# Performance work log

Hardware: AMD Instinct MI355X
Metric: run time of the kernel (lower is better)

The kernel has to match this reference:

```python
import jax, jax.numpy as jnp
import numpy as np

D_MODEL = 512
NHEAD = 8
HEAD_DIM = D_MODEL // NHEAD
D_FF = 2048
EPS = 1e-5


def _linear_params(key, d_in, d_out):
    kw, kb = jax.random.split(key)
    bound = 1.0 / np.sqrt(d_in)
    W = jax.random.uniform(kw, (d_out, d_in), jnp.float32, -bound, bound)
    b = jax.random.uniform(kb, (d_out,), jnp.float32, -bound, bound)
    return W, b


def setup_inputs() -> dict:
    key = jax.random.key(0)
    ks = jax.random.split(key, 8)
    src = jax.random.normal(ks[0], (4, 2048, D_MODEL), jnp.float32)
    Wq, bq = _linear_params(ks[1], D_MODEL, D_MODEL)
    Wk, bk = _linear_params(ks[2], D_MODEL, D_MODEL)
    Wv, bv = _linear_params(ks[3], D_MODEL, D_MODEL)
    Wo, bo = _linear_params(ks[4], D_MODEL, D_MODEL)
    W1, b1 = _linear_params(ks[5], D_MODEL, D_FF)
    W2, b2 = _linear_params(ks[6], D_FF, D_MODEL)
    g1 = jnp.ones((D_MODEL,), jnp.float32)
    be1 = jnp.zeros((D_MODEL,), jnp.float32)
    g2 = jnp.ones((D_MODEL,), jnp.float32)
    be2 = jnp.zeros((D_MODEL,), jnp.float32)
    return dict(src=src, Wq=Wq, bq=bq, Wk=Wk, bk=bk, Wv=Wv, bv=bv,
                Wo=Wo, bo=bo, W1=W1, b1=b1, W2=W2, b2=b2,
                g1=g1, be1=be1, g2=g2, be2=be2)


def _layer_norm(x, g, b):
    mu = jnp.mean(x, axis=-1, keepdims=True)
    var = jnp.mean(jnp.square(x - mu), axis=-1, keepdims=True)
    return (x - mu) / jnp.sqrt(var + EPS) * g + b


def reference(src, Wq, bq, Wk, bk, Wv, bv, Wo, bo, W1, b1, W2, b2, g1, be1, g2, be2):
    B, T, D = src.shape
    scale = np.sqrt(HEAD_DIM).astype(np.float32)
    # Projections (torch Linear: x @ W.T + b)
    Q = (src @ Wq.T + bq).reshape(B, T, NHEAD, HEAD_DIM).transpose(0, 2, 1, 3)
    K = (src @ Wk.T + bk).reshape(B, T, NHEAD, HEAD_DIM).transpose(0, 2, 1, 3)
    V = (src @ Wv.T + bv).reshape(B, T, NHEAD, HEAD_DIM).transpose(0, 2, 1, 3)
    # Explicit QK^T -> softmax -> V (no mask, dropout=0)
    scores = jnp.einsum('bhqd,bhkd->bhqk', Q, K) / scale  # (B,H,T,T)
    attn = jax.nn.softmax(scores, axis=-1)
    ctx = jnp.einsum('bhqk,bhkd->bhqd', attn, V)
    ctx = ctx.transpose(0, 2, 1, 3).reshape(B, T, D)
    attn_out = ctx @ Wo.T + bo
    # Add & Norm 1
    x = _layer_norm(src + attn_out, g1, be1)
    # FFN: Linear -> GELU -> Linear
    h = jax.nn.gelu(x @ W1.T + b1, approximate=False)
    ffn_out = h @ W2.T + b2
    # Add & Norm 2
    return _layer_norm(x + ffn_out, g2, be2)
```

## Files before the change

### kernel.cpp

```cpp
#include <hip/hip_runtime.h>
#include <hip/hip_bf16.h>
#include <hip/hip_fp16.h>
#include <math.h>

typedef __bf16 bf16_t;
typedef __bf16 bf16x8 __attribute__((ext_vector_type(8)));
typedef __bf16 bf16x2 __attribute__((ext_vector_type(2)));
typedef float  f32x4  __attribute__((ext_vector_type(4)));

#define D_MODEL 512
#define NHEAD   8
#define HD      64
#define D_FF    2048
#define TOKENS  8192
#define SEQ     2048
#define BATCH   4

__device__ __forceinline__ void gload16(const bf16_t* g, bf16_t* l)
{
    __builtin_amdgcn_global_load_lds(
        (const __attribute__((address_space(1))) void*)g,
        (__attribute__((address_space(3))) void*)l,
        16, 0, 0);
}

__device__ __forceinline__ void cvt4(const float* s, bf16_t* d)
{
    float4 v = *(const float4*)s;
    alignas(8) bf16_t t[4] = {(bf16_t)v.x, (bf16_t)v.y, (bf16_t)v.z, (bf16_t)v.w};
    *(uint2*)d = *(const uint2*)t;
}

__global__ void cvt_weights(const float* __restrict__ src,
                            const float* __restrict__ Wq, const float* __restrict__ Wk,
                            const float* __restrict__ Wv, const float* __restrict__ Wo,
                            const float* __restrict__ W1, const float* __restrict__ W2,
                            const float* __restrict__ bq, const float* __restrict__ bk,
                            const float* __restrict__ bv,
                            bf16_t* __restrict__ Xb,
                            bf16_t* __restrict__ Wqkvb, bf16_t* __restrict__ Wob,
                            bf16_t* __restrict__ W1b, bf16_t* __restrict__ W2b,
                            float* __restrict__ bqkv, float* __restrict__ zbias)
{
    int i = blockIdx.x * 256 + threadIdx.x;
    if (i < 1048576) { cvt4(src + (size_t)i * 4, Xb + (size_t)i * 4); return; }
    i -= 1048576;
    if (i < 65536)        cvt4(Wq + (size_t)i * 4,            Wqkvb + (size_t)i * 4);
    else if (i < 131072)  cvt4(Wk + (size_t)(i - 65536) * 4,  Wqkvb + (size_t)i * 4);
    else if (i < 196608)  cvt4(Wv + (size_t)(i - 131072) * 4, Wqkvb + (size_t)i * 4);
    else if (i < 262144)  cvt4(Wo + (size_t)(i - 196608) * 4, Wob + (size_t)(i - 196608) * 4);
    else if (i < 524288)  cvt4(W1 + (size_t)(i - 262144) * 4, W1b + (size_t)(i - 262144) * 4);
    else if (i < 786432)  cvt4(W2 + (size_t)(i - 524288) * 4, W2b + (size_t)(i - 524288) * 4);
    else if (i < 786816) {
        int j = i - 786432;
        const float* s = (j < 128) ? bq + j * 4 : (j < 256) ? bk + (j - 128) * 4
                                                            : bv + (j - 256) * 4;
        *(float4*)(bqkv + (j & 127) * 4 + (j >> 7) * 512) = *(const float4*)s;
    } else if (i < 786944) {
        int j = i - 786816;
        *(float4*)(zbias + j * 4) = make_float4(0.f, 0.f, 0.f, 0.f);
    }
}

template <int BM, int EPI, bool SPLIT2>
__global__ __launch_bounds__(256)
void gemm_bt(const bf16_t* __restrict__ A, const bf16_t* __restrict__ B,
             const float* __restrict__ bias, const float* __restrict__ biasz,
             void* __restrict__ Cout, int M, int N, int K)
{
    constexpr int MI = BM / 32;
    __shared__ bf16_t sA[2][BM][32];
    __shared__ bf16_t sB[2][128][32];
    bf16_t* sAf = &sA[0][0][0];
    bf16_t* sBf = &sB[0][0][0];

    const int tid  = threadIdx.x;
    const int wave = tid >> 6;
    const int lane = tid & 63;
    const int g    = lane >> 4;
    const int c16  = lane & 15;
    const int wm   = (wave >> 1) * (BM / 2);
    const int wn   = (wave & 1) * 64;
    const int m0   = blockIdx.y * BM;
    const int n0   = blockIdx.x * 128;

    const int zz    = SPLIT2 ? blockIdx.z : 0;
    const int Keff  = SPLIT2 ? (K >> 1) : K;
    const int kbase = zz * Keff;
    const float* bptr = (SPLIT2 && zz) ? biasz : bias;

    const f32x4 fz = {0.f, 0.f, 0.f, 0.f};
    f32x4 acc[MI][4];
#pragma unroll
    for (int i = 0; i < MI; i++)
#pragma unroll
        for (int j = 0; j < 4; j++) acc[i][j] = fz;

    const int srow = tid >> 2;
    const int scol = (tid & 3) * 8;
    const bf16_t* pa = A + (size_t)(m0 + srow) * K + kbase + scol;
    const bf16_t* pb = B + (size_t)(n0 + srow) * K + kbase + scol;

#pragma unroll
    for (int i = 0; i < BM / 64; i++)
        gload16(pa + (size_t)i * 64 * K, sAf + i * 2048 + tid * 8);
#pragma unroll
    for (int i = 0; i < 2; i++)
        gload16(pb + (size_t)i * 64 * K, sBf + i * 2048 + tid * 8);

    const int NK = Keff >> 5;
    for (int kk = 0; kk < NK; ++kk) {
        const int cur = kk & 1;
        __syncthreads();
        if (kk + 1 < NK) {
            const int k0 = (kk + 1) * 32;
            bf16_t* dA = sAf + (cur ^ 1) * (BM * 32);
            bf16_t* dB = sBf + (cur ^ 1) * 4096;
#pragma unroll
            for (int i = 0; i < BM / 64; i++)
                gload16(pa + (size_t)i * 64 * K + k0, dA + i * 2048 + tid * 8);
#pragma unroll
            for (int i = 0; i < 2; i++)
                gload16(pb + (size_t)i * 64 * K + k0, dB + i * 2048 + tid * 8);
        }

        bf16x8 af[MI], bfr[4];
#pragma unroll
        for (int i = 0; i < MI; i++)
            af[i] = *(const bf16x8*)&sA[cur][wm + i * 16 + c16][g * 8];
#pragma unroll
        for (int j = 0; j < 4; j++)
            bfr[j] = *(const bf16x8*)&sB[cur][wn + j * 16 + c16][g * 8];
#pragma unroll
        for (int mi = 0; mi < MI; mi++)
#pragma unroll
            for (int ni = 0; ni < 4; ni++)
                acc[mi][ni] = __builtin_amdgcn_mfma_f32_16x16x32_bf16(
                    af[mi], bfr[ni], acc[mi][ni], 0, 0, 0);
    }

    __half* outh = (__half*)Cout + (size_t)zz * M * N;
#pragma unroll
    for (int mi = 0; mi < MI; mi++) {
#pragma unroll
        for (int ni = 0; ni < 4; ni++) {
            const int col = n0 + wn + ni * 16 + c16;
            const float bv = bptr[col];
#pragma unroll
            for (int r = 0; r < 4; r++) {
                const int row = m0 + wm + mi * 16 + g * 4 + r;
                float v = acc[mi][ni][r] + bv;
                if (EPI == 1) v = 0.5f * v * (1.f + erff(v * 0.70710678118654752f));
                if (EPI == 2)
                    outh[(size_t)row * N + col] = (__half)v;
                else
                    ((bf16_t*)Cout)[(size_t)row * N + col] = (bf16_t)v;
            }
        }
    }
}

__global__ __launch_bounds__(256)
void transpose_v(const bf16_t* __restrict__ qkv, bf16_t* __restrict__ vt)
{
    __shared__ bf16_t st[64][72];
    const int t0 = blockIdx.x * 64;
    const int bh = blockIdx.y;
    const int b = bh >> 3, h = bh & 7;
    const int tid = threadIdx.x;

    for (int c = tid; c < 512; c += 256) {
        int r = c >> 3, cj = (c & 7) * 8;
        const bf16_t* src = qkv + ((size_t)(b * SEQ + t0 + r)) * 1536 + 1024 + h * 64 + cj;
        *(int4*)&st[r][cj] = *(const int4*)src;
    }
    __syncthreads();
    for (int c = tid; c < 512; c += 256) {
        int d = c >> 3, pj = (c & 7) * 8;
        alignas(16) bf16_t tmp[8];
#pragma unroll
        for (int j = 0; j < 8; j++) {
            int p = pj + j;
            int t = (p & 32) + ((p & 1) << 4) + ((p & 31) >> 1);
            tmp[j] = st[t][d];
        }
        *(int4*)(vt + ((size_t)(bh * 64 + d)) * SEQ + t0 + pj) = *(const int4*)tmp;
    }
}

__global__ __launch_bounds__(256)
void flash_attn(const bf16_t* __restrict__ qkv, const bf16_t* __restrict__ vt,
                bf16_t* __restrict__ ctx)
{
    __shared__ bf16_t sK[2][64][64];
    __shared__ bf16_t sVt[2][64][64];
    __shared__ bf16_t sP[128][64];

    const int bh = blockIdx.y;
    const int b = bh >> 3, h = bh & 7;
    const int q0 = blockIdx.x * 128;
    const int tid = threadIdx.x;
    const int wave = tid >> 6, lane = tid & 63;
    const int g = lane >> 4, c16 = lane & 15;

    const float qscale = 0.125f * 1.4426950408889634f;
    bf16x8 aq[2][2];
#pragma unroll
    for (int mf = 0; mf < 2; mf++)
#pragma unroll
        for (int ks = 0; ks < 2; ks++) {
            bf16x8 v = *(const bf16x8*)(qkv +
                ((size_t)(b * SEQ + q0 + wave * 32 + mf * 16 + c16)) * 1536 +
                h * 64 + ks * 32 + g * 8);
#pragma unroll
            for (int j = 0; j < 8; j++) v[j] = (bf16_t)((float)v[j] * qscale);
            aq[mf][ks] = v;
        }

    bf16x8 vb_ones;
    {
        const bf16_t o = (bf16_t)((c16 == 0) ? 1.0f : 0.0f);
#pragma unroll
        for (int j = 0; j < 8; j++) vb_ones[j] = o;
    }

    const f32x4 fz = {0.f, 0.f, 0.f, 0.f};
    f32x4 acc_o[2][5];
#pragma unroll
    for (int mf = 0; mf < 2; mf++)
#pragma unroll
        for (int nd = 0; nd < 5; nd++) acc_o[mf][nd] = fz;

    const int f0 = tid,        r0 = f0 >> 3, l0 = (f0 & 7) ^ (r0 & 7);
    const int f1 = tid + 256,  r1 = f1 >> 3, l1 = (f1 & 7) ^ (r1 & 7);
    const bf16_t* gK0 = qkv + ((size_t)(b * SEQ + r0)) * 1536 + 512 + h * 64 + l0 * 8;
    const bf16_t* gK1 = qkv + ((size_t)(b * SEQ + r1)) * 1536 + 512 + h * 64 + l1 * 8;
    const bf16_t* gV0 = vt + ((size_t)(bh * 64 + r0)) * SEQ + l0 * 8;
    const bf16_t* gV1 = vt + ((size_t)(bh * 64 + r1)) * SEQ + l1 * 8;
    bf16_t* lK = &sK[0][0][0];
    bf16_t* lV = &sVt[0][0][0];

    gload16(gK0, lK + f0 * 8);
    gload16(gK1, lK + f1 * 8);
    gload16(gV0, lV + f0 * 8);
    gload16(gV1, lV + f1 * 8);

    for (int it = 0; it < 32; ++it) {
        const int cur = it & 1;
        __syncthreads();
        if (it < 31) {
            const size_t kv = (size_t)(it + 1) * 64;
            const int bo = (cur ^ 1) * 4096;
            gload16(gK0 + kv * 1536, lK + bo + f0 * 8);
            gload16(gK1 + kv * 1536, lK + bo + f1 * 8);
            gload16(gV0 + kv,        lV + bo + f0 * 8);
            gload16(gV1 + kv,        lV + bo + f1 * 8);
        }

        f32x4 accs[2][4];
#pragma unroll
        for (int mf = 0; mf < 2; mf++)
#pragma unroll
            for (int n = 0; n < 4; n++) accs[mf][n] = fz;
#pragma unroll
        for (int ks = 0; ks < 2; ks++)
#pragma unroll
            for (int n = 0; n < 4; n++) {
                const int pc = ((ks * 4 + g) ^ (c16 & 7)) * 8;
                bf16x8 bk = *(const bf16x8*)&sK[cur][n * 16 + c16][pc];
                accs[0][n] = __builtin_amdgcn_mfma_f32_16x16x32_bf16(aq[0][ks], bk, accs[0][n], 0, 0, 0);
                accs[1][n] = __builtin_amdgcn_mfma_f32_16x16x32_bf16(aq[1][ks], bk, accs[1][n], 0, 0, 0);
            }

#pragma unroll
        for (int mf = 0; mf < 2; mf++)
#pragma unroll
            for (int r = 0; r < 4; r++) {
                const int prow = wave * 32 + mf * 16 + g * 4 + r;
#pragma unroll
                for (int ks = 0; ks < 2; ks++) {
                    bf16x2 pp;
                    pp[0] = (bf16_t)__builtin_amdgcn_exp2f(accs[mf][2 * ks][r]);
                    pp[1] = (bf16_t)__builtin_amdgcn_exp2f(accs[mf][2 * ks + 1][r]);
                    const int lc = ks * 4 + (c16 >> 2);
                    const int pc = ((lc ^ (prow & 7)) << 3) + ((2 * c16) & 7);
                    *(bf16x2*)&sP[prow][pc] = pp;
                }
            }

#pragma unroll
        for (int ks = 0; ks < 2; ks++) {
            const int rpc = ((ks * 4 + g) ^ (c16 & 7)) * 8;
            bf16x8 ap0 = *(const bf16x8*)&sP[wave * 32 + c16][rpc];
            bf16x8 ap1 = *(const bf16x8*)&sP[wave * 32 + 16 + c16][rpc];
#pragma unroll
            for (int nd = 0; nd < 5; nd++) {
                bf16x8 vb;
                if (nd < 4) {
                    const int pc = ((ks * 4 + g) ^ (c16 & 7)) * 8;
                    vb = *(const bf16x8*)&sVt[cur][nd * 16 + c16][pc];
                } else {
                    vb = vb_ones;
                }
                acc_o[0][nd] = __builtin_amdgcn_mfma_f32_16x16x32_bf16(ap0, vb, acc_o[0][nd], 0, 0, 0);
                acc_o[1][nd] = __builtin_amdgcn_mfma_f32_16x16x32_bf16(ap1, vb, acc_o[1][nd], 0, 0, 0);
            }
        }
    }

#pragma unroll
    for (int mf = 0; mf < 2; mf++)
#pragma unroll
        for (int r = 0; r < 4; r++) {
            float lv  = __shfl(acc_o[mf][4][r], lane & 48, 64);
            float inv = 1.0f / lv;
            const size_t base =
                ((size_t)(b * SEQ + q0 + wave * 32 + mf * 16 + g * 4 + r)) * 512 + h * 64;
#pragma unroll
            for (int nd = 0; nd < 4; nd++)
                ctx[base + nd * 16 + c16] = (bf16_t)(acc_o[mf][nd][r] * inv);
        }
}

__global__ __launch_bounds__(256)
void add_ln3(const float* __restrict__ a, const __half* __restrict__ b,
             const __half* __restrict__ c,
             const float* __restrict__ gamma, const float* __restrict__ beta,
             float* __restrict__ outf, bf16_t* __restrict__ outb)
{
    const int row  = blockIdx.x * 4 + (threadIdx.x >> 6);
    const int lane = threadIdx.x & 63;
    const size_t base = (size_t)row * 512 + lane * 8;

    int4 braw = *(const int4*)(b + base);
    int4 craw = *(const int4*)(c + base);
    const __half* bh = (const __half*)&braw;
    const __half* ch = (const __half*)&craw;

    float v[8];
#pragma unroll
    for (int hh = 0; hh < 2; hh++) {
        float4 av = *(const float4*)(a + base + hh * 4);
        v[hh * 4 + 0] = av.x + (float)bh[hh * 4 + 0] + (float)ch[hh * 4 + 0];
        v[hh * 4 + 1] = av.y + (float)bh[hh * 4 + 1] + (float)ch[hh * 4 + 1];
        v[hh * 4 + 2] = av.z + (float)bh[hh * 4 + 2] + (float)ch[hh * 4 + 2];
        v[hh * 4 + 3] = av.w + (float)bh[hh * 4 + 3] + (float)ch[hh * 4 + 3];
    }

    float s = 0.f;
#pragma unroll
    for (int i = 0; i < 8; i++) s += v[i];
#pragma unroll
    for (int off = 32; off > 0; off >>= 1) s += __shfl_xor(s, off);
    const float mu = s * (1.f / 512.f);

    float q = 0.f;
#pragma unroll
    for (int i = 0; i < 8; i++) { float d = v[i] - mu; q += d * d; }
#pragma unroll
    for (int off = 32; off > 0; off >>= 1) q += __shfl_xor(q, off);
    const float rstd = rsqrtf(q * (1.f / 512.f) + 1e-5f);

    float4 g0 = *(const float4*)(gamma + lane * 8);
    float4 g1 = *(const float4*)(gamma + lane * 8 + 4);
    float4 e0 = *(const float4*)(beta + lane * 8);
    float4 e1 = *(const float4*)(beta + lane * 8 + 4);
    const float gg[8] = {g0.x, g0.y, g0.z, g0.w, g1.x, g1.y, g1.z, g1.w};
    const float ee[8] = {e0.x, e0.y, e0.z, e0.w, e1.x, e1.y, e1.z, e1.w};

    float o[8];
#pragma unroll
    for (int i = 0; i < 8; i++) o[i] = (v[i] - mu) * rstd * gg[i] + ee[i];

    *(float4*)(outf + base)     = make_float4(o[0], o[1], o[2], o[3]);
    *(float4*)(outf + base + 4) = make_float4(o[4], o[5], o[6], o[7]);
    if (outb) {
        alignas(16) bf16_t ob[8];
#pragma unroll
        for (int i = 0; i < 8; i++) ob[i] = (bf16_t)o[i];
        *(int4*)(outb + base) = *(const int4*)ob;
    }
}

extern "C" void kernel_launch(void* const* d_in, const int* in_sizes, int n_in,
                              void* d_out, int out_size, void* d_ws, size_t ws_size,
                              hipStream_t stream)
{
    const float* src = (const float*)d_in[0];
    const float* Wq  = (const float*)d_in[1];  const float* bq  = (const float*)d_in[2];
    const float* Wk  = (const float*)d_in[3];  const float* bk  = (const float*)d_in[4];
    const float* Wv  = (const float*)d_in[5];  const float* bv  = (const float*)d_in[6];
    const float* Wo  = (const float*)d_in[7];  const float* bo  = (const float*)d_in[8];
    const float* W1  = (const float*)d_in[9];  const float* b1  = (const float*)d_in[10];
    const float* W2  = (const float*)d_in[11]; const float* b2  = (const float*)d_in[12];
    const float* g1  = (const float*)d_in[13]; const float* be1 = (const float*)d_in[14];
    const float* g2  = (const float*)d_in[15]; const float* be2 = (const float*)d_in[16];
    float* out = (float*)d_out;

    char* ws = (char*)d_ws;
    size_t off = 0;
    auto alloc = [&](size_t bytes) -> void* {
        void* p = ws + off;
        off = (off + bytes + 255) & ~(size_t)255;
        return p;
    };

    bf16_t* Xb    = (bf16_t*)alloc((size_t)TOKENS * 512 * 2);
    bf16_t* Wqkvb = (bf16_t*)alloc((size_t)1536 * 512 * 2);
    bf16_t* Wob   = (bf16_t*)alloc((size_t)512 * 512 * 2);
    bf16_t* W1b   = (bf16_t*)alloc((size_t)2048 * 512 * 2);
    bf16_t* W2b   = (bf16_t*)alloc((size_t)512 * 2048 * 2);
    float*  bqkv  = (float*)alloc(1536 * 4);
    float*  zbias = (float*)alloc(512 * 4);
    bf16_t* QKV   = (bf16_t*)alloc((size_t)TOKENS * 1536 * 2);
    bf16_t* Vt    = (bf16_t*)alloc((size_t)32 * 64 * SEQ * 2);
    bf16_t* CTX   = (bf16_t*)alloc((size_t)TOKENS * 512 * 2);
    __half* ATTa  = (__half*)alloc((size_t)TOKENS * 512 * 2);
    __half* ATTb  = (__half*)alloc((size_t)TOKENS * 512 * 2);
    float*  X1    = (float*)alloc((size_t)TOKENS * 512 * 4);
    bf16_t* X1b   = (bf16_t*)alloc((size_t)TOKENS * 512 * 2);

    bf16_t* H    = QKV;
    __half* FFNa = ATTa;
    __half* FFNb = ATTb;

    cvt_weights<<<7170, 256, 0, stream>>>(src, Wq, Wk, Wv, Wo, W1, W2, bq, bk, bv,
                                          Xb, Wqkvb, Wob, W1b, W2b, bqkv, zbias);

    gemm_bt<128, 0, false><<<dim3(12, 64), 256, 0, stream>>>(
        Xb, Wqkvb, bqkv, zbias, QKV, TOKENS, 1536, 512);

    transpose_v<<<dim3(32, 32), 256, 0, stream>>>(QKV, Vt);
    flash_attn<<<dim3(16, 32), 256, 0, stream>>>(QKV, Vt, CTX);

    gemm_bt<64, 2, true><<<dim3(4, 128, 2), 256, 0, stream>>>(
        CTX, Wob, bo, zbias, ATTa, TOKENS, 512, 512);

    add_ln3<<<2048, 256, 0, stream>>>(src, ATTa, ATTb, g1, be1, X1, X1b);

    gemm_bt<128, 1, false><<<dim3(16, 64), 256, 0, stream>>>(
        X1b, W1b, b1, zbias, H, TOKENS, 2048, 512);

    gemm_bt<64, 2, true><<<dim3(4, 128, 2), 256, 0, stream>>>(
        H, W2b, b2, zbias, FFNa, TOKENS, 512, 2048);

    add_ln3<<<2048, 256, 0, stream>>>(X1, FFNa, FFNb, g2, be2, out, nullptr);
}
```

Before: 286.1 us.

## Compute transposed attention tiles so probabilities stay in registers, removing sP LDS round-trip

```diff
diff --git a/kernel.cpp b/kernel.cpp
--- a/kernel.cpp
+++ b/kernel.cpp
@@ -181,7 +181,7 @@
 #pragma unroll
         for (int j = 0; j < 8; j++) {
             int p = pj + j;
-            int t = (p & 32) + ((p & 1) << 4) + ((p & 31) >> 1);
+            int t = ((p >> 5) << 5) + (((p >> 2) & 1) << 4) + (((p >> 3) & 3) << 2) + (p & 3);
             tmp[j] = st[t][d];
         }
         *(int4*)(vt + ((size_t)(bh * 64 + d)) * SEQ + t0 + pj) = *(const int4*)tmp;
@@ -189,12 +189,12 @@
 }
 
 __global__ __launch_bounds__(256)
+__attribute__((amdgpu_waves_per_eu(2, 2)))
 void flash_attn(const bf16_t* __restrict__ qkv, const bf16_t* __restrict__ vt,
                 bf16_t* __restrict__ ctx)
 {
     __shared__ bf16_t sK[2][64][64];
     __shared__ bf16_t sVt[2][64][64];
-    __shared__ bf16_t sP[128][64];
 
     const int bh = blockIdx.y;
     const int b = bh >> 3, h = bh & 7;
@@ -206,30 +206,24 @@
     const float qscale = 0.125f * 1.4426950408889634f;
     bf16x8 aq[2][2];
 #pragma unroll
-    for (int mf = 0; mf < 2; mf++)
+    for (int qt = 0; qt < 2; qt++)
 #pragma unroll
         for (int ks = 0; ks < 2; ks++) {
             bf16x8 v = *(const bf16x8*)(qkv +
-                ((size_t)(b * SEQ + q0 + wave * 32 + mf * 16 + c16)) * 1536 +
+                ((size_t)(b * SEQ + q0 + wave * 32 + qt * 16 + c16)) * 1536 +
                 h * 64 + ks * 32 + g * 8);
 #pragma unroll
             for (int j = 0; j < 8; j++) v[j] = (bf16_t)((float)v[j] * qscale);
-            aq[mf][ks] = v;
-        }
-
-    bf16x8 vb_ones;
-    {
-        const bf16_t o = (bf16_t)((c16 == 0) ? 1.0f : 0.0f);
-#pragma unroll
-        for (int j = 0; j < 8; j++) vb_ones[j] = o;
-    }
+            aq[qt][ks] = v;
+        }
 
     const f32x4 fz = {0.f, 0.f, 0.f, 0.f};
-    f32x4 acc_o[2][5];
-#pragma unroll
-    for (int mf = 0; mf < 2; mf++)
-#pragma unroll
-        for (int nd = 0; nd < 5; nd++) acc_o[mf][nd] = fz;
+    f32x4 acc_oT[4][2];
+#pragma unroll
+    for (int dt = 0; dt < 4; dt++)
+#pragma unroll
+        for (int qt = 0; qt < 2; qt++) acc_oT[dt][qt] = fz;
+    float l_acc[2] = {0.f, 0.f};
 
     const int f0 = tid,        r0 = f0 >> 3, l0 = (f0 & 7) ^ (r0 & 7);
     const int f1 = tid + 256,  r1 = f1 >> 3, l1 = (f1 & 7) ^ (r1 & 7);
@@ -257,69 +251,72 @@
             gload16(gV1 + kv,        lV + bo + f1 * 8);
         }
 
-        f32x4 accs[2][4];
-#pragma unroll
-        for (int mf = 0; mf < 2; mf++)
-#pragma unroll
-            for (int n = 0; n < 4; n++) accs[mf][n] = fz;
-#pragma unroll
-        for (int ks = 0; ks < 2; ks++)
-#pragma unroll
-            for (int n = 0; n < 4; n++) {
-                const int pc = ((ks * 4 + g) ^ (c16 & 7)) * 8;
-                bf16x8 bk = *(const bf16x8*)&sK[cur][n * 16 + c16][pc];
-                accs[0][n] = __builtin_amdgcn_mfma_f32_16x16x32_bf16(aq[0][ks], bk, accs[0][n], 0, 0, 0);
-                accs[1][n] = __builtin_amdgcn_mfma_f32_16x16x32_bf16(aq[1][ks], bk, accs[1][n], 0, 0, 0);
+        f32x4 accs[4][2];
+#pragma unroll
+        for (int tt = 0; tt < 4; tt++)
+#pragma unroll
+            for (int qt = 0; qt < 2; qt++) accs[tt][qt] = fz;
+#pragma unroll
+        for (int ks = 0; ks < 2; ks++) {
+            const int pc = ((ks * 4 + g) ^ (c16 & 7)) * 8;
+#pragma unroll
+            for (int tt = 0; tt < 4; tt++) {
+                bf16x8 ak = *(const bf16x8*)&sK[cur][tt * 16 + c16][pc];
+                accs[tt][0] = __builtin_amdgcn_mfma_f32_16x16x32_bf16(ak, aq[0][ks], accs[tt][0], 0, 0, 0);
+                accs[tt][1] = __builtin_amdgcn_mfma_f32_16x16x32_bf16(ak, aq[1][ks], accs[tt][1], 0, 0, 0);
             }
-
-#pragma unroll
-        for (int mf = 0; mf < 2; mf++)
-#pragma unroll
-            for (int r = 0; r < 4; r++) {
-                const int prow = wave * 32 + mf * 16 + g * 4 + r;
-#pragma unroll
-                for (int ks = 0; ks < 2; ks++) {
-                    bf16x2 pp;
-                    pp[0] = (bf16_t)__builtin_amdgcn_exp2f(accs[mf][2 * ks][r]);
-                    pp[1] = (bf16_t)__builtin_amdgcn_exp2f(accs[mf][2 * ks + 1][r]);
-                    const int lc = ks * 4 + (c16 >> 2);
-                    const int pc = ((lc ^ (prow & 7)) << 3) + ((2 * c16) & 7);
-                    *(bf16x2*)&sP[prow][pc] = pp;
+        }
+
+#pragma unroll
+        for (int tt = 0; tt < 4; tt++)
+#pragma unroll
+            for (int qt = 0; qt < 2; qt++) {
+                float s = 0.f;
+#pragma unroll
+                for (int r = 0; r < 4; r++) {
+                    float p = __builtin_amdgcn_exp2f(accs[tt][qt][r]);
+                    accs[tt][qt][r] = p;
+                    s += p;
                 }
+                l_acc[qt] += s;
             }
-
-#pragma unroll
-        for (int ks = 0; ks < 2; ks++) {
-            const int rpc = ((ks * 4 + g) ^ (c16 & 7)) * 8;
-            bf16x8 ap0 = *(const bf16x8*)&sP[wave * 32 + c16][rpc];
-            bf16x8 ap1 = *(const bf16x8*)&sP[wave * 32 + 16 + c16][rpc];
-#pragma unroll
-            for (int nd = 0; nd < 5; nd++) {
-                bf16x8 vb;
-                if (nd < 4) {
-                    const int pc = ((ks * 4 + g) ^ (c16 & 7)) * 8;
-                    vb = *(const bf16x8*)&sVt[cur][nd * 16 + c16][pc];
-                } else {
-                    vb = vb_ones;
-                }
-                acc_o[0][nd] = __builtin_amdgcn_mfma_f32_16x16x32_bf16(ap0, vb, acc_o[0][nd], 0, 0, 0);
-                acc_o[1][nd] = __builtin_amdgcn_mfma_f32_16x16x32_bf16(ap1, vb, acc_o[1][nd], 0, 0, 0);
+        bf16x8 pb[2][2];
+#pragma unroll
+        for (int qt = 0; qt < 2; qt++)
+#pragma unroll
+            for (int kv = 0; kv < 2; kv++)
+#pragma unroll
+                for (int j = 0; j < 8; j++)
+                    pb[qt][kv][j] = (bf16_t)accs[kv * 2 + (j >> 2)][qt][j & 3];
+
+#pragma unroll
+        for (int kv = 0; kv < 2; kv++) {
+            const int pc = ((kv * 4 + g) ^ (c16 & 7)) * 8;
+#pragma unroll
+            for (int dt = 0; dt < 4; dt++) {
+                bf16x8 av = *(const bf16x8*)&sVt[cur][dt * 16 + c16][pc];
+                acc_oT[dt][0] = __builtin_amdgcn_mfma_f32_16x16x32_bf16(av, pb[0][kv], acc_oT[dt][0], 0, 0, 0);
+                acc_oT[dt][1] = __builtin_amdgcn_mfma_f32_16x16x32_bf16(av, pb[1][kv], acc_oT[dt][1], 0, 0, 0);
             }
         }
     }
 
 #pragma unroll
-    for (int mf = 0; mf < 2; mf++)
-#pragma unroll
-        for (int r = 0; r < 4; r++) {
-            float lv  = __shfl(acc_o[mf][4][r], lane & 48, 64);
-            float inv = 1.0f / lv;
-            const size_t base =
-                ((size_t)(b * SEQ + q0 + wave * 32 + mf * 16 + g * 4 + r)) * 512 + h * 64;
-#pragma unroll
-            for (int nd = 0; nd < 4; nd++)
-                ctx[base + nd * 16 + c16] = (bf16_t)(acc_o[mf][nd][r] * inv);
-        }
+    for (int qt = 0; qt < 2; qt++) {
+        float l = l_acc[qt];
+        l += __shfl_xor(l, 16);
+        l += __shfl_xor(l, 32);
+        const float inv = 1.0f / l;
+        const int token = q0 + wave * 32 + qt * 16 + c16;
+        bf16_t* dst = ctx + ((size_t)(b * SEQ + token)) * 512 + h * 64 + g * 4;
+#pragma unroll
+        for (int dt = 0; dt < 4; dt++) {
+            alignas(8) bf16_t o4[4];
+#pragma unroll
+            for (int r = 0; r < 4; r++) o4[r] = (bf16_t)(acc_oT[dt][qt][r] * inv);
+            *(uint2*)(dst + dt * 16) = *(const uint2*)o4;
+        }
+    }
 }
 
 __global__ __launch_bounds__(256)
```

Measured after the change: 281.3 us. Within noise of the previous version (-1.7%).
